# Kernel tuning notes

Hardware: AMD Instinct MI355X
Metric: run time of the kernel (lower is better)

The kernel has to match this reference:

```python
import jax, jax.numpy as jnp
import numpy as np

B, T, C, H, DH = 2, 2048, 768, 12, 64


def setup_inputs() -> dict:
    key = jax.random.key(0)
    k1, k2, k3 = jax.random.split(key, 3)
    x = jax.random.normal(k1, (B, T, C), dtype=jnp.float32)
    Wqkv = jax.random.normal(k2, (C, 3 * C), dtype=jnp.float32) * (C ** -0.5)
    Wout = jax.random.normal(k3, (C, C), dtype=jnp.float32) * (C ** -0.5)
    return {"x": x, "Wqkv": Wqkv, "Wout": Wout}


def reference(x, Wqkv, Wout):
    b, t, c = x.shape
    qkv = x @ Wqkv  # [B,T,3C]
    q, k, v = jnp.split(qkv, 3, axis=-1)
    # [B,T,C] -> [B,H,T,dh]
    q = q.reshape(b, t, H, DH).transpose(0, 2, 1, 3)
    k = k.reshape(b, t, H, DH).transpose(0, 2, 1, 3)
    v = v.reshape(b, t, H, DH).transpose(0, 2, 1, 3)
    scale = DH ** -0.5
    scores = jnp.einsum('bhqd,bhkd->bhqk', q, k) * scale  # [B,H,T,T]
    causal = jnp.tril(jnp.ones((t, t), dtype=bool))
    scores = jnp.where(causal, scores, -jnp.inf)
    weights = jax.nn.softmax(scores, axis=-1)
    # dropout p=0.0 -> identity
    out = jnp.einsum('bhqk,bhkd->bhqd', weights, v)  # [B,H,T,dh]
    out = out.transpose(0, 2, 1, 3).reshape(b, t, c)
    return out @ Wout
```

## Files before the change

kernel.cpp:

```cpp
#include <hip/hip_runtime.h>
#include <hip/hip_bf16.h>

#define Bn 2
#define Tn 2048
#define Cn 768
#define Hn 12
#define Dn 64
#define N3n 2304
#define Mn 4096

#define MASKVAL (-30000.f)
#define NITEMS 1152
#define DEFER_THR 64.f
#define L2E8 0.1803368801111204f

typedef unsigned short u16;
typedef __attribute__((ext_vector_type(8))) unsigned short ushort8_t;
typedef __attribute__((ext_vector_type(8))) short bf16x8;
typedef __attribute__((ext_vector_type(4))) float f32x4;
typedef __attribute__((address_space(1))) unsigned int* gas1_t;
typedef __attribute__((address_space(3))) unsigned int* las3_t;

__device__ __forceinline__ float bf2f(u16 u) {
  union { unsigned int i; float f; } v; v.i = ((unsigned int)u) << 16; return v.f;
}
__device__ __forceinline__ u16 f2bf(float f) {
  union { float f; unsigned int i; } v; v.f = f;
  return (u16)((v.i + 0x7fffu + ((v.i >> 16) & 1u)) >> 16);
}

#define E(qt, s0, s1, ck) (((qt) << 24) | ((s0) << 16) | ((s1) << 8) | (ck))
__constant__ unsigned int SCHED[48] = {
    E(31, 0, 16, 0), E(31, 16, 32, 1), E(30, 0, 16, 0), E(15, 0, 16, 2),
    E(30, 16, 31, 1), E(29, 0, 15, 0), E(29, 15, 30, 1), E(28, 0, 15, 0), E(14, 0, 15, 2),
    E(28, 15, 29, 1), E(27, 0, 14, 0), E(27, 14, 28, 1), E(26, 0, 14, 0), E(13, 0, 14, 2),
    E(26, 14, 27, 1), E(25, 0, 13, 0), E(25, 13, 26, 1), E(24, 0, 13, 0), E(12, 0, 13, 2),
    E(24, 13, 25, 1), E(23, 0, 12, 0), E(23, 12, 24, 1), E(22, 0, 12, 0), E(11, 0, 12, 2),
    E(22, 12, 23, 1), E(21, 0, 11, 0), E(21, 11, 22, 1), E(20, 0, 11, 0), E(10, 0, 11, 2),
    E(20, 11, 21, 1), E(19, 0, 10, 0), E(19, 10, 20, 1), E(18, 0, 10, 0), E(9, 0, 10, 2),
    E(18, 10, 19, 1), E(17, 0, 9, 0), E(17, 9, 18, 1), E(16, 0, 9, 0), E(8, 0, 9, 2),
    E(16, 9, 17, 1), E(7, 0, 8, 2),
    E(6, 0, 7, 2), E(5, 0, 6, 2), E(4, 0, 5, 2), E(3, 0, 4, 2), E(2, 0, 3, 2),
    E(1, 0, 2, 2), E(0, 0, 1, 2)};

__global__ __launch_bounds__(256) void cast_bf16(const float* __restrict__ in,
                                                 u16* __restrict__ out,
                                                 int* __restrict__ counter) {
  if (blockIdx.x == 0 && threadIdx.x == 0) *counter = 0;
  const int i = (blockIdx.x * 256 + threadIdx.x) * 4;
  float4 v = *(const float4*)(in + i);
  ushort4 s;
  s.x = f2bf(v.x); s.y = f2bf(v.y); s.z = f2bf(v.z); s.w = f2bf(v.w);
  *(ushort4*)(out + i) = s;
}

__global__ __launch_bounds__(256) void transpose_cast_w(const float* __restrict__ Wqkv,
                                                        const float* __restrict__ Wout,
                                                        u16* __restrict__ WqkvT,
                                                        u16* __restrict__ WoutT) {
  __shared__ u16 t[32][33];
  const bool isA = blockIdx.x < (N3n / 32);
  const float* in = isA ? Wqkv : Wout;
  u16* out = isA ? WqkvT : WoutT;
  const int Cc = isA ? N3n : Cn;
  const int c0 = (isA ? blockIdx.x : blockIdx.x - N3n / 32) * 32;
  const int r0 = blockIdx.y * 32;
  const int tx = threadIdx.x, ty = threadIdx.y;
#pragma unroll
  for (int i = 0; i < 4; i++)
    t[ty * 4 + i][tx] = f2bf(in[(size_t)(r0 + ty * 4 + i) * Cc + c0 + tx]);
  __syncthreads();
#pragma unroll
  for (int i = 0; i < 4; i++)
    out[(size_t)(c0 + ty * 4 + i) * Cn + r0 + tx] = t[tx][ty * 4 + i];
}

#define BK 64

template <int EPI>
__global__ __launch_bounds__(256) void mfma_gemm(const u16* __restrict__ A,
                                                 const u16* __restrict__ BT,
                                                 u16* __restrict__ Q,
                                                 u16* __restrict__ Kd,
                                                 u16* __restrict__ VT,
                                                 float* __restrict__ out) {
  __shared__ __align__(16) u16 Ash[128 * BK];
  __shared__ __align__(16) u16 Bsh[128 * BK];
  const int tid = threadIdx.x;
  const int wv = tid >> 6, lane = tid & 63;
  const int lo = lane & 15, quad = lane >> 4;
  const int wm = wv & 1, wn = wv >> 1;

  const int nwg = gridDim.x * gridDim.y;
  const int cpx = nwg >> 3;
  const int lid = blockIdx.y * gridDim.x + blockIdx.x;
  const int swz = (lid & 7) * cpx + (lid >> 3);
  const int n0 = (swz % gridDim.x) * 128;
  const int m0 = (swz / gridDim.x) * 128;

  const int srow = lane >> 3;
  const int scol = (lane & 7) << 3;

  f32x4 acc[4][4];
#pragma unroll
  for (int i = 0; i < 4; i++)
#pragma unroll
    for (int j = 0; j < 4; j++) acc[i][j] = f32x4{0.f, 0.f, 0.f, 0.f};

  for (int k0 = 0; k0 < Cn; k0 += BK) {
    __syncthreads();
#pragma unroll
    for (int c = 0; c < 4; c++) {
      const int rb = (wv << 5) + (c << 3);
      const int gr = rb + srow;
      __builtin_amdgcn_global_load_lds(
          (gas1_t)(A + (size_t)(m0 + gr) * Cn + k0 + scol),
          (las3_t)(&Ash[rb * BK]), 16, 0, 0);
      __builtin_amdgcn_global_load_lds(
          (gas1_t)(BT + (size_t)(n0 + gr) * Cn + k0 + scol),
          (las3_t)(&Bsh[rb * BK]), 16, 0, 0);
    }
    __syncthreads();

    bf16x8 af[4][2], bfr[4][2];
#pragma unroll
    for (int t = 0; t < 4; t++) {
#pragma unroll
      for (int s = 0; s < 2; s++) {
        af[t][s]  = *(const bf16x8*)&Ash[(wm * 64 + t * 16 + lo) * BK + s * 32 + (quad << 3)];
        bfr[t][s] = *(const bf16x8*)&Bsh[(wn * 64 + t * 16 + lo) * BK + s * 32 + (quad << 3)];
      }
    }
#pragma unroll
    for (int mt = 0; mt < 4; mt++)
#pragma unroll
      for (int nt = 0; nt < 4; nt++) {
        acc[mt][nt] = __builtin_amdgcn_mfma_f32_16x16x32_bf16(af[mt][0], bfr[nt][0],
                                                              acc[mt][nt], 0, 0, 0);
        acc[mt][nt] = __builtin_amdgcn_mfma_f32_16x16x32_bf16(af[mt][1], bfr[nt][1],
                                                              acc[mt][nt], 0, 0, 0);
      }
  }

  if (EPI == 0) {
    const int which = n0 / Cn;
    const int h = ((n0 % Cn) >> 6) + wn;
    const int bb = m0 >> 11;
    const int t_base = (m0 & (Tn - 1)) + wm * 64;
    if (which < 2) {
      u16* dst = ((which == 0) ? Q : Kd) + (size_t)(bb * Hn + h) * Tn * Dn;
#pragma unroll
      for (int mt = 0; mt < 4; mt++)
#pragma unroll
        for (int nt = 0; nt < 4; nt++)
#pragma unroll
          for (int r = 0; r < 4; r++) {
            const int t = t_base + mt * 16 + (quad << 2) + r;
            dst[(size_t)t * Dn + nt * 16 + lo] = f2bf(acc[mt][nt][r]);
          }
    } else {
      u16* dst = VT + (size_t)(bb * Hn + h) * Dn * Tn;
#pragma unroll
      for (int mt = 0; mt < 4; mt++)
#pragma unroll
        for (int nt = 0; nt < 4; nt++) {
          const int t = t_base + mt * 16 + (quad << 2);
          const int d = nt * 16 + lo;
          ushort4 st;
          st.x = f2bf(acc[mt][nt][0]); st.y = f2bf(acc[mt][nt][1]);
          st.z = f2bf(acc[mt][nt][2]); st.w = f2bf(acc[mt][nt][3]);
          *(ushort4*)&dst[(size_t)d * Tn + t] = st;
        }
    }
  } else {
#pragma unroll
    for (int mt = 0; mt < 4; mt++)
#pragma unroll
      for (int nt = 0; nt < 4; nt++)
#pragma unroll
        for (int r = 0; r < 4; r++) {
          const int m = m0 + wm * 64 + mt * 16 + (quad << 2) + r;
          out[(size_t)m * Cn + n0 + wn * 64 + nt * 16 + lo] = acc[mt][nt][r];
        }
  }
}

#define KP 72
#define TILE_W (64 * KP)

__global__ __launch_bounds__(256) void attn_kernel(const u16* __restrict__ Q,
                                                   const u16* __restrict__ K,
                                                   const u16* __restrict__ VT,
                                                   u16* __restrict__ O,
                                                   int* __restrict__ counter,
                                                   float* __restrict__ po,
                                                   float* __restrict__ pm,
                                                   float* __restrict__ pl) {
  __shared__ __align__(16) u16 Ksh[2 * TILE_W];
  __shared__ __align__(16) u16 Vsh[2 * TILE_W];
  __shared__ __align__(16) u16 Pw[4][16 * KP];
  __shared__ int s_item;

  const int tid = threadIdx.x;
  const int wv = tid >> 6, lane = tid & 63;
  const int lo = lane & 15, quad = lane >> 4;
  const int sr = tid >> 3;
  const int sc = (tid & 7) << 3;

  for (;;) {
    if (tid == 0) s_item = atomicAdd(counter, 1);
    __syncthreads();
    const int item = s_item;
    if (item >= NITEMS) return;

    const unsigned int e = SCHED[item / 24];
    const int qt = e >> 24, ck = e & 255;
    const int jstart = ((e >> 16) & 255) << 6;
    const int jend   = ((e >> 8) & 255) << 6;
    const int q0 = qt << 6;
    const int hb = item % 24;
    const int h = hb % 12, b = hb / 12;
    const size_t base = (size_t)(b * Hn + h) * Tn * Dn;
    const size_t vtb  = (size_t)(b * Hn + h) * Dn * Tn;

    const u16* qp = Q + base + (size_t)(q0 + (wv << 4) + lo) * Dn + (quad << 3);
    const bf16x8 aq0 = *(const bf16x8*)qp;
    const bf16x8 aq1 = *(const bf16x8*)(qp + 32);

    f32x4 o[4] = {f32x4{0,0,0,0}, f32x4{0,0,0,0}, f32x4{0,0,0,0}, f32x4{0,0,0,0}};
    float m1 = MASKVAL;
    float l1 = 0.f;

#pragma unroll
    for (int it = 0; it < 2; it++) {
      const int r = sr + it * 32;
      *(ushort8_t*)&Ksh[r * KP + sc] =
          *(const ushort8_t*)(K + base + (size_t)(jstart + r) * Dn + sc);
      *(ushort8_t*)&Vsh[r * KP + sc] =
          *(const ushort8_t*)(VT + vtb + (size_t)r * Tn + jstart + sc);
    }
    __syncthreads();

    int cur = 0;
    const int qrel = (wv << 4) + lo;

    for (int j0 = jstart; j0 < jend; j0 += 64) {
      const bool hasnext = (j0 + 64 < jend);

      ushort8_t kr[2], vr[2];
      if (hasnext) {
#pragma unroll
        for (int it = 0; it < 2; it++) {
          const int r = sr + it * 32;
          kr[it] = *(const ushort8_t*)(K + base + (size_t)(j0 + 64 + r) * Dn + sc);
          vr[it] = *(const ushort8_t*)(VT + vtb + (size_t)r * Tn + j0 + 64 + sc);
        }
      }

      const u16* Kb_ = &Ksh[cur * TILE_W];
      const u16* Vb_ = &Vsh[cur * TILE_W];

      f32x4 s[4];
#pragma unroll
      for (int nt = 0; nt < 4; nt++) {
        const bf16x8 bk0 = *(const bf16x8*)(&Kb_[(nt * 16 + lo) * KP + (quad << 3)]);
        const bf16x8 bk1 = *(const bf16x8*)(&Kb_[(nt * 16 + lo) * KP + 32 + (quad << 3)]);
        f32x4 a = {0.f, 0.f, 0.f, 0.f};
        a = __builtin_amdgcn_mfma_f32_16x16x32_bf16(bk0, aq0, a, 0, 0, 0);
        a = __builtin_amdgcn_mfma_f32_16x16x32_bf16(bk1, aq1, a, 0, 0, 0);
        s[nt] = a;
      }

      if (j0 == q0) {
#pragma unroll
        for (int nt = 0; nt < 4; nt++)
#pragma unroll
          for (int r = 0; r < 4; r++) {
            const int kv = nt * 16 + (quad << 2) + r;
            if (kv > qrel) s[nt][r] = MASKVAL;
          }
      }

      float mx = fmaxf(s[0][0], s[0][1]);
      mx = fmaxf(fmaxf(mx, s[0][2]), s[0][3]);
      mx = fmaxf(fmaxf(mx, s[1][0]), s[1][1]);
      mx = fmaxf(fmaxf(mx, s[1][2]), s[1][3]);
      mx = fmaxf(fmaxf(mx, s[2][0]), s[2][1]);
      mx = fmaxf(fmaxf(mx, s[2][2]), s[2][3]);
      mx = fmaxf(fmaxf(mx, s[3][0]), s[3][1]);
      mx = fmaxf(fmaxf(mx, s[3][2]), s[3][3]);
      const float pmax = mx;

      if (!__all(pmax <= m1 + DEFER_THR)) {
        float mr = fmaxf(pmax, __shfl_xor(pmax, 16));
        mr = fmaxf(mr, __shfl_xor(mr, 32));
        const float mnew = fmaxf(m1, mr);
        const float alpha = __builtin_amdgcn_exp2f(L2E8 * (m1 - mnew));
        m1 = mnew;
        l1 *= alpha;
        float ar[4];
#pragma unroll
        for (int r = 0; r < 4; r++) ar[r] = __shfl(alpha, (quad << 2) + r);
#pragma unroll
        for (int nt = 0; nt < 4; nt++)
#pragma unroll
          for (int r = 0; r < 4; r++) o[nt][r] *= ar[r];
      }

      const float mb2 = L2E8 * m1;
      float sum = 0.f;
#pragma unroll
      for (int nt = 0; nt < 4; nt++)
#pragma unroll
        for (int r = 0; r < 4; r++) {
          const float p = __builtin_amdgcn_exp2f(L2E8 * s[nt][r] - mb2);
          s[nt][r] = p;
          sum += p;
        }
      l1 += sum;

      u16* pw = Pw[wv];
#pragma unroll
      for (int nt = 0; nt < 4; nt++) {
        ushort4 pk;
        pk.x = f2bf(s[nt][0]); pk.y = f2bf(s[nt][1]);
        pk.z = f2bf(s[nt][2]); pk.w = f2bf(s[nt][3]);
        *(ushort4*)&pw[lo * KP + nt * 16 + (quad << 2)] = pk;
      }
      const bf16x8 pa0 = *(const bf16x8*)(&pw[lo * KP + (quad << 3)]);
      const bf16x8 pa1 = *(const bf16x8*)(&pw[lo * KP + 32 + (quad << 3)]);

#pragma unroll
      for (int nt = 0; nt < 4; nt++) {
        const bf16x8 bv0 = *(const bf16x8*)(&Vb_[(nt * 16 + lo) * KP + (quad << 3)]);
        const bf16x8 bv1 = *(const bf16x8*)(&Vb_[(nt * 16 + lo) * KP + 32 + (quad << 3)]);
        o[nt] = __builtin_amdgcn_mfma_f32_16x16x32_bf16(pa0, bv0, o[nt], 0, 0, 0);
        o[nt] = __builtin_amdgcn_mfma_f32_16x16x32_bf16(pa1, bv1, o[nt], 0, 0, 0);
      }

      if (hasnext) {
        const int nb = cur ^ 1;
#pragma unroll
        for (int it = 0; it < 2; it++) {
          const int r = sr + it * 32;
          *(ushort8_t*)&Ksh[nb * TILE_W + r * KP + sc] = kr[it];
          *(ushort8_t*)&Vsh[nb * TILE_W + r * KP + sc] = vr[it];
        }
      }
      __syncthreads();
      cur ^= 1;
    }

    float lt = l1;
    lt += __shfl_xor(lt, 16);
    lt += __shfl_xor(lt, 32);
    const float linv = 1.f / lt;
    float ir[4];
#pragma unroll
    for (int r = 0; r < 4; r++) ir[r] = __shfl(linv, (quad << 2) + r);

    if (ck == 2) {
#pragma unroll
      for (int nt = 0; nt < 4; nt++)
#pragma unroll
        for (int r = 0; r < 4; r++) {
          const int row = q0 + (wv << 4) + (quad << 2) + r;
          const int col = h * 64 + nt * 16 + lo;
          O[(size_t)(b * Tn + row) * Cn + col] = f2bf(o[nt][r] * ir[r]);
        }
    } else {
      const int st = hb * 16 + (qt - 16);
      const int pidx = st * 2 + ck;
      float* pO = po + ((size_t)pidx << 12);
#pragma unroll
      for (int nt = 0; nt < 4; nt++)
#pragma unroll
        for (int r = 0; r < 4; r++)
          pO[((wv << 4) + (quad << 2) + r) * 64 + nt * 16 + lo] = o[nt][r] * ir[r];
      if (quad == 0) {
        pm[pidx * 64 + (wv << 4) + lo] = m1;
        pl[pidx * 64 + (wv << 4) + lo] = lt;
      }
    }
  }
}

__global__ __launch_bounds__(256) void combine_kernel(const float* __restrict__ po,
                                                      const float* __restrict__ pm,
                                                      const float* __restrict__ pl,
                                                      u16* __restrict__ O) {
  const int st = blockIdx.x;
  const int hb = st >> 4;
  const int h = hb % 12, b = hb / 12;
  const int q0 = (16 + (st & 15)) << 6;
  const int tid = threadIdx.x;
  const int row = tid >> 2, cc0 = (tid & 3) << 4;
  const float* pa = po + (((size_t)st * 2) << 12) + row * 64 + cc0;
  const float* pb = pa + 4096;
  const float ma = pm[st * 128 + row],      la = pl[st * 128 + row];
  const float mb = pm[st * 128 + 64 + row], lb = pl[st * 128 + 64 + row];
  const float mm = fmaxf(ma, mb);
  float wa = la * __builtin_amdgcn_exp2f(L2E8 * (ma - mm));
  float wb = lb * __builtin_amdgcn_exp2f(L2E8 * (mb - mm));
  const float wi = 1.f / (wa + wb);
  wa *= wi; wb *= wi;
  u16* Orow = O + (size_t)(b * Tn + q0 + row) * Cn + h * 64 + cc0;
#pragma unroll
  for (int i = 0; i < 16; i += 4) {
    const float4 va = *(const float4*)(pa + i);
    const float4 vb = *(const float4*)(pb + i);
    ushort4 s4;
    s4.x = f2bf(wa * va.x + wb * vb.x);
    s4.y = f2bf(wa * va.y + wb * vb.y);
    s4.z = f2bf(wa * va.z + wb * vb.z);
    s4.w = f2bf(wa * va.w + wb * vb.w);
    *(ushort4*)(Orow + i) = s4;
  }
}

extern "C" void kernel_launch(void* const* d_in, const int* in_sizes, int n_in,
                              void* d_out, int out_size, void* d_ws, size_t ws_size,
                              hipStream_t stream) {
  const float* x    = (const float*)d_in[0];
  const float* Wqkv = (const float*)d_in[1];
  const float* Wout = (const float*)d_in[2];
  float* out = (float*)d_out;

  const size_t per = (size_t)Bn * Hn * Tn * Dn;
  u16* xb    = (u16*)d_ws;
  u16* WqkvT = xb + (size_t)Mn * Cn;
  u16* WoutT = WqkvT + (size_t)N3n * Cn;
  u16* Qb    = WoutT + (size_t)Cn * Cn;
  u16* Kb    = Qb + per;
  u16* VTb   = Kb + per;
  u16* attn  = VTb + per;
  int* counter = (int*)(attn + (size_t)Mn * Cn);
  float* po = (float*)(counter + 512);
  float* pm = po + (size_t)768 * 4096;
  float* pl = pm + (size_t)768 * 64;

  cast_bf16<<<(Mn * Cn) / 1024, 256, 0, stream>>>(x, xb, counter);
  transpose_cast_w<<<dim3(N3n / 32 + Cn / 32, Cn / 32), dim3(32, 8), 0, stream>>>(
      Wqkv, Wout, WqkvT, WoutT);

  mfma_gemm<0><<<dim3(N3n / 128, Mn / 128), 256, 0, stream>>>(xb, WqkvT, Qb, Kb, VTb, nullptr);
  attn_kernel<<<dim3(768), 256, 0, stream>>>(Qb, Kb, VTb, attn, counter, po, pm, pl);
  combine_kernel<<<dim3(384), 256, 0, stream>>>(po, pm, pl, attn);
  mfma_gemm<1><<<dim3(Cn / 128, Mn / 128), 256, 0, stream>>>(attn, WoutT, nullptr, nullptr, nullptr, out);
}
```

Baseline: 184.9 us.

## Swizzle attention LDS tiles, raise occupancy, and merge prep kernels

Replaces the padded LDS rows (stride 72) in the attention kernel with unpadded 64-wide rows using an XOR swizzle on 16-byte chunks for K, V and P tiles. This avoids bank conflicts without padding. The work-item slot is moved into the K buffer. The smaller LDS footprint lets more blocks be resident, and the persistent grid grows from 768 to 1024 blocks. The two input cast/transpose kernels are fused into one launch to cut launch overhead. The risk is that aliasing the item slot with the K buffer depends on synchronization ordering.

```diff
diff --git a/kernel.cpp b/kernel.cpp
--- a/kernel.cpp
+++ b/kernel.cpp
@@ -43,36 +43,41 @@
     E(6, 0, 7, 2), E(5, 0, 6, 2), E(4, 0, 5, 2), E(3, 0, 4, 2), E(2, 0, 3, 2),
     E(1, 0, 2, 2), E(0, 0, 1, 2)};
 
-__global__ __launch_bounds__(256) void cast_bf16(const float* __restrict__ in,
-                                                 u16* __restrict__ out,
-                                                 int* __restrict__ counter) {
-  if (blockIdx.x == 0 && threadIdx.x == 0) *counter = 0;
-  const int i = (blockIdx.x * 256 + threadIdx.x) * 4;
-  float4 v = *(const float4*)(in + i);
-  ushort4 s;
-  s.x = f2bf(v.x); s.y = f2bf(v.y); s.z = f2bf(v.z); s.w = f2bf(v.w);
-  *(ushort4*)(out + i) = s;
-}
-
-__global__ __launch_bounds__(256) void transpose_cast_w(const float* __restrict__ Wqkv,
-                                                        const float* __restrict__ Wout,
-                                                        u16* __restrict__ WqkvT,
-                                                        u16* __restrict__ WoutT) {
+__global__ __launch_bounds__(256) void prep_kernel(const float* __restrict__ x,
+                                                   const float* __restrict__ Wqkv,
+                                                   const float* __restrict__ Wout,
+                                                   u16* __restrict__ xb,
+                                                   u16* __restrict__ WqkvT,
+                                                   u16* __restrict__ WoutT,
+                                                   int* __restrict__ counter) {
   __shared__ u16 t[32][33];
-  const bool isA = blockIdx.x < (N3n / 32);
-  const float* in = isA ? Wqkv : Wout;
-  u16* out = isA ? WqkvT : WoutT;
-  const int Cc = isA ? N3n : Cn;
-  const int c0 = (isA ? blockIdx.x : blockIdx.x - N3n / 32) * 32;
-  const int r0 = blockIdx.y * 32;
-  const int tx = threadIdx.x, ty = threadIdx.y;
-#pragma unroll
-  for (int i = 0; i < 4; i++)
-    t[ty * 4 + i][tx] = f2bf(in[(size_t)(r0 + ty * 4 + i) * Cc + c0 + tx]);
-  __syncthreads();
-#pragma unroll
-  for (int i = 0; i < 4; i++)
-    out[(size_t)(c0 + ty * 4 + i) * Cn + r0 + tx] = t[tx][ty * 4 + i];
+  const int bx = blockIdx.x;
+  const int tid = threadIdx.x;
+  if (bx < 3072) {
+    if (bx == 0 && tid == 0) *counter = 0;
+    const int i = (bx * 256 + tid) * 4;
+    float4 v = *(const float4*)(x + i);
+    ushort4 s;
+    s.x = f2bf(v.x); s.y = f2bf(v.y); s.z = f2bf(v.z); s.w = f2bf(v.w);
+    *(ushort4*)(xb + i) = s;
+  } else {
+    const int idx = bx - 3072;
+    const int gx = idx % 96, gy = idx / 96;
+    const bool isA = gx < (N3n / 32);
+    const float* in = isA ? Wqkv : Wout;
+    u16* out = isA ? WqkvT : WoutT;
+    const int Cc = isA ? N3n : Cn;
+    const int c0 = (isA ? gx : gx - N3n / 32) * 32;
+    const int r0 = gy * 32;
+    const int tx = tid & 31, ty = tid >> 5;
+#pragma unroll
+    for (int i = 0; i < 4; i++)
+      t[ty * 4 + i][tx] = f2bf(in[(size_t)(r0 + ty * 4 + i) * Cc + c0 + tx]);
+    __syncthreads();
+#pragma unroll
+    for (int i = 0; i < 4; i++)
+      out[(size_t)(c0 + ty * 4 + i) * Cn + r0 + tx] = t[tx][ty * 4 + i];
+  }
 }
 
 #define BK 64
@@ -185,8 +190,7 @@
   }
 }
 
-#define KP 72
-#define TILE_W (64 * KP)
+#define TILE_W (64 * 64)
 
 __global__ __launch_bounds__(256) void attn_kernel(const u16* __restrict__ Q,
                                                    const u16* __restrict__ K,
@@ -198,19 +202,23 @@
                                                    float* __restrict__ pl) {
   __shared__ __align__(16) u16 Ksh[2 * TILE_W];
   __shared__ __align__(16) u16 Vsh[2 * TILE_W];
-  __shared__ __align__(16) u16 Pw[4][16 * KP];
-  __shared__ int s_item;
+  __shared__ __align__(16) u16 Pw[4][16 * 64];
+  int* sip = (int*)&Ksh[TILE_W];
 
   const int tid = threadIdx.x;
   const int wv = tid >> 6, lane = tid & 63;
   const int lo = lane & 15, quad = lane >> 4;
+  const int lo7 = lo & 7;
+  const int ck0 = (quad ^ lo7) << 3;
+  const int ck1 = ck0 ^ 32;
   const int sr = tid >> 3;
   const int sc = (tid & 7) << 3;
+  const int scw = (((tid & 7) ^ (sr & 7)) << 3);
 
   for (;;) {
-    if (tid == 0) s_item = atomicAdd(counter, 1);
+    if (tid == 0) *sip = atomicAdd(counter, 1);
     __syncthreads();
-    const int item = s_item;
+    const int item = *sip;
     if (item >= NITEMS) return;
 
     const unsigned int e = SCHED[item / 24];
@@ -234,9 +242,9 @@
 #pragma unroll
     for (int it = 0; it < 2; it++) {
       const int r = sr + it * 32;
-      *(ushort8_t*)&Ksh[r * KP + sc] =
+      *(ushort8_t*)&Ksh[r * 64 + scw] =
           *(const ushort8_t*)(K + base + (size_t)(jstart + r) * Dn + sc);
-      *(ushort8_t*)&Vsh[r * KP + sc] =
+      *(ushort8_t*)&Vsh[r * 64 + scw] =
           *(const ushort8_t*)(VT + vtb + (size_t)r * Tn + jstart + sc);
     }
     __syncthreads();
@@ -263,8 +271,8 @@
       f32x4 s[4];
 #pragma unroll
       for (int nt = 0; nt < 4; nt++) {
-        const bf16x8 bk0 = *(const bf16x8*)(&Kb_[(nt * 16 + lo) * KP + (quad << 3)]);
-        const bf16x8 bk1 = *(const bf16x8*)(&Kb_[(nt * 16 + lo) * KP + 32 + (quad << 3)]);
+        const bf16x8 bk0 = *(const bf16x8*)(&Kb_[(nt * 16 + lo) * 64 + ck0]);
+        const bf16x8 bk1 = *(const bf16x8*)(&Kb_[(nt * 16 + lo) * 64 + ck1]);
         f32x4 a = {0.f, 0.f, 0.f, 0.f};
         a = __builtin_amdgcn_mfma_f32_16x16x32_bf16(bk0, aq0, a, 0, 0, 0);
         a = __builtin_amdgcn_mfma_f32_16x16x32_bf16(bk1, aq1, a, 0, 0, 0);
@@ -325,15 +333,16 @@
         ushort4 pk;
         pk.x = f2bf(s[nt][0]); pk.y = f2bf(s[nt][1]);
         pk.z = f2bf(s[nt][2]); pk.w = f2bf(s[nt][3]);
-        *(ushort4*)&pw[lo * KP + nt * 16 + (quad << 2)] = pk;
-      }
-      const bf16x8 pa0 = *(const bf16x8*)(&pw[lo * KP + (quad << 3)]);
-      const bf16x8 pa1 = *(const bf16x8*)(&pw[lo * KP + 32 + (quad << 3)]);
+        const int pc = (((2 * nt + (quad >> 1)) ^ lo7) << 3) + ((quad & 1) << 2);
+        *(ushort4*)&pw[lo * 64 + pc] = pk;
+      }
+      const bf16x8 pa0 = *(const bf16x8*)(&pw[lo * 64 + ck0]);
+      const bf16x8 pa1 = *(const bf16x8*)(&pw[lo * 64 + ck1]);
 
 #pragma unroll
       for (int nt = 0; nt < 4; nt++) {
-        const bf16x8 bv0 = *(const bf16x8*)(&Vb_[(nt * 16 + lo) * KP + (quad << 3)]);
-        const bf16x8 bv1 = *(const bf16x8*)(&Vb_[(nt * 16 + lo) * KP + 32 + (quad << 3)]);
+        const bf16x8 bv0 = *(const bf16x8*)(&Vb_[(nt * 16 + lo) * 64 + ck0]);
+        const bf16x8 bv1 = *(const bf16x8*)(&Vb_[(nt * 16 + lo) * 64 + ck1]);
         o[nt] = __builtin_amdgcn_mfma_f32_16x16x32_bf16(pa0, bv0, o[nt], 0, 0, 0);
         o[nt] = __builtin_amdgcn_mfma_f32_16x16x32_bf16(pa1, bv1, o[nt], 0, 0, 0);
       }
@@ -343,8 +352,8 @@
 #pragma unroll
         for (int it = 0; it < 2; it++) {
           const int r = sr + it * 32;
-          *(ushort8_t*)&Ksh[nb * TILE_W + r * KP + sc] = kr[it];
-          *(ushort8_t*)&Vsh[nb * TILE_W + r * KP + sc] = vr[it];
+          *(ushort8_t*)&Ksh[nb * TILE_W + r * 64 + scw] = kr[it];
+          *(ushort8_t*)&Vsh[nb * TILE_W + r * 64 + scw] = vr[it];
         }
       }
       __syncthreads();
@@ -439,12 +448,10 @@
   float* pm = po + (size_t)768 * 4096;
   float* pl = pm + (size_t)768 * 64;
 
-  cast_bf16<<<(Mn * Cn) / 1024, 256, 0, stream>>>(x, xb, counter);
-  transpose_cast_w<<<dim3(N3n / 32 + Cn / 32, Cn / 32), dim3(32, 8), 0, stream>>>(
-      Wqkv, Wout, WqkvT, WoutT);
-
+  prep_kernel<<<dim3(3072 + 2304), 256, 0, stream>>>(x, Wqkv, Wout, xb, WqkvT,
+                                                     WoutT, counter);
   mfma_gemm<0><<<dim3(N3n / 128, Mn / 128), 256, 0, stream>>>(xb, WqkvT, Qb, Kb, VTb, nullptr);
-  attn_kernel<<<dim3(768), 256, 0, stream>>>(Qb, Kb, VTb, attn, counter, po, pm, pl);
+  attn_kernel<<<dim3(1024), 256, 0, stream>>>(Qb, Kb, VTb, attn, counter, po, pm, pl);
   combine_kernel<<<dim3(384), 256, 0, stream>>>(po, pm, pl, attn);
   mfma_gemm<1><<<dim3(Cn / 128, Mn / 128), 256, 0, stream>>>(attn, WoutT, nullptr, nullptr, nullptr, out);
 }
```

New measurement: 184.4 us. About the same (-0.3%).
